# Optimization experiments

Measured on AMD Instinct MI355X. Metric: run time of the kernel, lower is better.

## Reference

```python
import jax, jax.numpy as jnp
import numpy as np

B, H, N, D = 1, 8, 2048, 64  # n >> d: fastmax's intended long-seq / small-head-dim regime


def setup_inputs() -> dict:
    key = jax.random.key(0)
    kq, kk, kv, kr = jax.random.split(key, 4)
    q = jax.random.normal(kq, (B, H, N, D), dtype=jnp.float32)
    k = jax.random.normal(kk, (B, H, N, D), dtype=jnp.float32)
    v = jax.random.normal(kv, (B, H, N, D), dtype=jnp.float32)
    rpe_matrix = jax.random.normal(kr, (2 * N - 1, D), dtype=jnp.float32)
    return {"q": q, "k": k, "v": v, "rpe_matrix": rpe_matrix, "mask": 1}


def reference(q, k, v, rpe_matrix, mask):
    # Fastmax: 2nd-order Taylor approximation of softmax attention,
    # weight(i,j) = 1 + s_ij + s_ij^2 / 2 where s_ij = q_i . (k_j) + q_i . rpe[i-j+n-1],
    # normalized by the row-sum, optionally causal (mask).
    b, h, n, d = q.shape
    # content scores: (b,h,n,n)
    s = jnp.einsum('bhid,bhjd->bhij', q, k)
    # RPE scores: project q onto every relative-position embedding, then gather
    # the (i,j) -> i-j+n-1 diagonal structure.  qr: (b,h,n,2n-1)
    qr = jnp.einsum('bhid,md->bhim', q, rpe_matrix)
    i = jnp.arange(n)[:, None]
    j = jnp.arange(n)[None, :]
    rel = i - j + (n - 1)  # (n,n) in [0, 2n-2]
    s = s + jnp.take_along_axis(qr, rel[None, None], axis=-1)
    # Taylor-2 exp approximation
    w = 1.0 + s + 0.5 * s * s
    if mask:  # causal
        w = jnp.where(j <= i, w, 0.0)
    denom = jnp.sum(w, axis=-1, keepdims=True)  # (b,h,n,1)
    out = jnp.einsum('bhij,bhjd->bhid', w, v) / denom
    return out
```

## Files before the change

### kernel.cpp

```cpp
#include <hip/hip_runtime.h>
#include <hip/hip_bf16.h>

#define HH 8
#define NN 2048
#define DD 64

typedef __attribute__((ext_vector_type(8))) short bf16x8;
typedef __attribute__((ext_vector_type(4))) float f32x4;
typedef __attribute__((ext_vector_type(8))) unsigned short u16x8;
typedef unsigned short ushort_t;

static __device__ __forceinline__ unsigned short f2bf(float x) {
    union { float f; unsigned u; } un; un.f = x;
    unsigned r = un.u + 0x7FFFu + ((un.u >> 16) & 1u);
    return (unsigned short)(r >> 16);
}
static __device__ __forceinline__ unsigned short f2bf_t(float x) {
    union { float f; unsigned u; } un; un.f = x;
    return (unsigned short)(un.u >> 16);
}
static __device__ __forceinline__ float bf2f(unsigned short u) {
    union { unsigned u; float f; } un; un.u = ((unsigned)u) << 16;
    return un.f;
}

#define OFF_Q  0u
#define OFF_K  2097152u
#define OFF_VT 4194304u
#define OFF_R  6291456u
#define OFF_P  6815744u
#define WS_NEED 11272192u

#define NQ4 262144
#define NR4 65520
#define CVT_BLOCKS 2305
__global__ void pre_kernel(const float* __restrict__ q, const float* __restrict__ k,
                           const float* __restrict__ r, const float* __restrict__ v,
                           ushort_t* __restrict__ ws) {
    __shared__ __align__(16) ushort_t T[64][72];
    if (blockIdx.x < CVT_BLOCKS) {
        int idx = blockIdx.x * 256 + threadIdx.x;
        const float* src; ushort_t* dst; int off;
        if (idx < NQ4) { src = q; dst = (ushort_t*)((char*)ws + OFF_Q); off = idx; }
        else if (idx < 2 * NQ4) { src = k; dst = (ushort_t*)((char*)ws + OFF_K); off = idx - NQ4; }
        else if (idx < 2 * NQ4 + NR4) { src = r; dst = (ushort_t*)((char*)ws + OFF_R); off = idx - 2 * NQ4; }
        else return;
        float4 f = *(const float4*)&src[4 * (size_t)off];
        ushort4 u; u.x = f2bf(f.x); u.y = f2bf(f.y); u.z = f2bf(f.z); u.w = f2bf(f.w);
        *(ushort4*)&dst[4 * (size_t)off] = u;
    } else {
        ushort_t* vt = (ushort_t*)((char*)ws + OFF_VT);
        const int bb = blockIdx.x - CVT_BLOCKS;
        const int h = bb >> 5;
        const int n0 = (bb & 31) * 64;
        const int tid = threadIdx.x;
        const float* vh = v + (size_t)h * NN * DD;
        #pragma unroll
        for (int p = 0; p < 4; ++p) {
            int c = tid + 256 * p; int rr = c >> 4, dc = (c & 15) << 2;
            float4 f = *(const float4*)&vh[(size_t)(n0 + rr) * DD + dc];
            T[dc + 0][rr] = f2bf(f.x); T[dc + 1][rr] = f2bf(f.y);
            T[dc + 2][rr] = f2bf(f.z); T[dc + 3][rr] = f2bf(f.w);
        }
        __syncthreads();
        #pragma unroll
        for (int p = 0; p < 2; ++p) {
            int c = tid + 256 * p; int d = c >> 3, nn = (c & 7) << 3;
            *(u16x8*)&vt[((size_t)h * 64 + d) * NN + n0 + nn] = *(const u16x8*)&T[d][nn];
        }
    }
}

__global__ __launch_bounds__(256, 2)
void fastmax_main(const ushort_t* __restrict__ wsb, float* __restrict__ outg,
                  float* __restrict__ wsPart)
{
    __shared__ __align__(16) ushort_t Ks[2][64][72];
    __shared__ __align__(16) ushort_t Bs[2][96][72];
    __shared__ __align__(16) ushort_t Vts[2][64][72];
    __shared__ __align__(16) unsigned char U[12800];
    float* Epi = (float*)U;

    const ushort_t* qb  = (const ushort_t*)((const char*)wsb + OFF_Q);
    const ushort_t* kb  = (const ushort_t*)((const char*)wsb + OFF_K);
    const ushort_t* vtb = (const ushort_t*)((const char*)wsb + OFF_VT);
    const ushort_t* rb_ = (const ushort_t*)((const char*)wsb + OFF_R);

    const int tid = threadIdx.x;
    const int w   = tid >> 6;
    const int l   = tid & 63;
    const int lq  = l >> 4;
    const int ln  = l & 15;
    const int rt  = w & 1;
    const int ch  = w >> 1;

    ushort_t* tsW = (ushort_t*)(U + w * 1920);
    ushort_t* wsW = (ushort_t*)(U + 7680 + w * 1280);

    const int sb     = blockIdx.x & 1;
    const int stream = blockIdx.x >> 1;
    const int head   = stream & 7;
    const int p      = stream >> 3;
    const int tileA  = 63 - p;
    const int njtA   = (tileA >> 1) + 1;
    const int tileB  = p;
    const int njtB   = (tileB >> 1) + 1;

    const ushort_t* qh  = qb  + (size_t)head * NN * DD;
    const ushort_t* kh  = kb  + (size_t)head * NN * DD;
    const ushort_t* vth = vtb + (size_t)head * DD * NN;
    float*          oh  = outg + (size_t)head * NN * DD;

    const int sw = 16 * rt - 32 * ch + 32;

    u16x8 rk0, rk1, rbA, rbB, rbC, rv0, rv1;
    const int c0r = tid >> 3,         c0d = (tid & 7) << 3;
    const int c1r = (tid + 256) >> 3, c1d = ((tid + 256) & 7) << 3;
    const int c2r = (tid + 512) >> 3, c2d = ((tid + 512) & 7) << 3;

    #pragma unroll 1
    for (int tsel = 0; tsel < 2; ++tsel) {
        if (tsel == 1 && sb == 0) break;
        const int tile = tsel ? tileB : tileA;
        const int jlo  = tsel ? 0 : (sb ? 17 : 0);
        const int jhi  = tsel ? njtB : (sb ? njtA : 17);
        const int i0   = tile * 32;

        bf16x8 qf0 = *(const bf16x8*)&qh[(size_t)(i0 + 16 * rt + ln) * DD +  0 + 8 * lq];
        bf16x8 qf1 = *(const bf16x8*)&qh[(size_t)(i0 + 16 * rt + ln) * DD + 32 + 8 * lq];

        f32x4 acc0 = {0,0,0,0}, acc1 = {0,0,0,0}, acc2 = {0,0,0,0}, acc3 = {0,0,0,0};
        float denv0 = 0.f, denv1 = 0.f, denv2 = 0.f, denv3 = 0.f;

        {
            const int j0 = jlo * 64;
            const int relbase = i0 - j0 + 1984;
            rk0 = *(const u16x8*)&kh[(size_t)(j0 + c0r) * DD + c0d];
            rk1 = *(const u16x8*)&kh[(size_t)(j0 + c1r) * DD + c1d];
            int r0 = relbase + c0r; if (r0 > 4094) r0 = 4094;
            int r1 = relbase + c1r; if (r1 > 4094) r1 = 4094;
            int r2 = relbase + c2r; if (r2 > 4094) r2 = 4094;
            rbA = *(const u16x8*)&rb_[(size_t)r0 * DD + c0d];
            rbB = *(const u16x8*)&rb_[(size_t)r1 * DD + c1d];
            rbC = *(const u16x8*)&rb_[(size_t)r2 * DD + c2d];
            rv0 = *(const u16x8*)&vth[(size_t)c0r * NN + j0 + c0d];
            rv1 = *(const u16x8*)&vth[(size_t)c1r * NN + j0 + c1d];
        }

        int buf = 0;
        for (int jt = jlo; jt < jhi; ++jt) {
            const int j0 = jt * 64;

            *(u16x8*)&Ks[buf][c0r][c0d] = rk0;
            *(u16x8*)&Ks[buf][c1r][c1d] = rk1;
            *(u16x8*)&Bs[buf][c0r][c0d] = rbA;
            *(u16x8*)&Bs[buf][c1r][c1d] = rbB;
            *(u16x8*)&Bs[buf][c2r][c2d] = rbC;
            *(u16x8*)&Vts[buf][c0r][c0d] = rv0;
            *(u16x8*)&Vts[buf][c1r][c1d] = rv1;

            if (jt + 1 < jhi) {
                const int jn = j0 + 64;
                const int relbase = i0 - jn + 1984;
                rk0 = *(const u16x8*)&kh[(size_t)(jn + c0r) * DD + c0d];
                rk1 = *(const u16x8*)&kh[(size_t)(jn + c1r) * DD + c1d];
                int r0 = relbase + c0r; if (r0 > 4094) r0 = 4094;
                int r1 = relbase + c1r; if (r1 > 4094) r1 = 4094;
                int r2 = relbase + c2r; if (r2 > 4094) r2 = 4094;
                rbA = *(const u16x8*)&rb_[(size_t)r0 * DD + c0d];
                rbB = *(const u16x8*)&rb_[(size_t)r1 * DD + c1d];
                rbC = *(const u16x8*)&rb_[(size_t)r2 * DD + c2d];
                rv0 = *(const u16x8*)&vth[(size_t)c0r * NN + jn + c0d];
                rv1 = *(const u16x8*)&vth[(size_t)c1r * NN + jn + c1d];
            }

            __syncthreads();

            f32x4 s0 = {0,0,0,0}, s1 = {0,0,0,0};
            {
                bf16x8 b00 = *(const bf16x8*)&Ks[buf][32 * ch      + ln][ 0 + 8 * lq];
                bf16x8 b01 = *(const bf16x8*)&Ks[buf][32 * ch      + ln][32 + 8 * lq];
                bf16x8 b10 = *(const bf16x8*)&Ks[buf][32 * ch + 16 + ln][ 0 + 8 * lq];
                bf16x8 b11 = *(const bf16x8*)&Ks[buf][32 * ch + 16 + ln][32 + 8 * lq];
                s0 = __builtin_amdgcn_mfma_f32_16x16x32_bf16(qf0, b00, s0, 0, 0, 0);
                s0 = __builtin_amdgcn_mfma_f32_16x16x32_bf16(qf1, b01, s0, 0, 0, 0);
                s1 = __builtin_amdgcn_mfma_f32_16x16x32_bf16(qf0, b10, s1, 0, 0, 0);
                s1 = __builtin_amdgcn_mfma_f32_16x16x32_bf16(qf1, b11, s1, 0, 0, 0);
            }

            #pragma unroll
            for (int bt = 0; bt < 3; ++bt) {
                f32x4 t = {0,0,0,0};
                bf16x8 b0 = *(const bf16x8*)&Bs[buf][sw + 16 * bt + ln][ 0 + 8 * lq];
                bf16x8 b1 = *(const bf16x8*)&Bs[buf][sw + 16 * bt + ln][32 + 8 * lq];
                t = __builtin_amdgcn_mfma_f32_16x16x32_bf16(qf0, b0, t, 0, 0, 0);
                t = __builtin_amdgcn_mfma_f32_16x16x32_bf16(qf1, b1, t, 0, 0, 0);
                ushort4 pk;
                pk.x = f2bf_t(t[0]); pk.y = f2bf_t(t[1]);
                pk.z = f2bf_t(t[2]); pk.w = f2bf_t(t[3]);
                *(ushort4*)&tsW[(16 * bt + ln) * 20 + 4 * lq] = pk;
            }

            #pragma unroll
            for (int ct = 0; ct < 2; ++ct) {
                f32x4 sv = ct ? s1 : s0;
                #pragma unroll
                for (int e = 0; e < 4; ++e) {
                    int rp = 4 * lq + e;
                    int cp = 16 * ct + ln;
                    int bw = rp - cp + 31;
                    float s = sv[e] + bf2f(tsW[bw * 20 + rp]);
                    float wv = 1.0f + s + 0.5f * s * s;
                    if (j0 + 32 * ch + cp > i0 + 16 * rt + rp) wv = 0.0f;
                    union { float f; unsigned u; } uw; uw.f = wv;
                    wsW[rp * 40 + cp] = (ushort_t)(uw.u >> 16);
                    uw.u &= 0xffff0000u;
                    if (e == 0) denv0 += uw.f; else if (e == 1) denv1 += uw.f;
                    else if (e == 2) denv2 += uw.f; else denv3 += uw.f;
                }
            }

            {
                bf16x8 af = *(const bf16x8*)&wsW[ln * 40 + 8 * lq];
                bf16x8 b;
                b = *(const bf16x8*)&Vts[buf][ 0 + ln][32 * ch + 8 * lq];
                acc0 = __builtin_amdgcn_mfma_f32_16x16x32_bf16(af, b, acc0, 0, 0, 0);
                b = *(const bf16x8*)&Vts[buf][16 + ln][32 * ch + 8 * lq];
                acc1 = __builtin_amdgcn_mfma_f32_16x16x32_bf16(af, b, acc1, 0, 0, 0);
                b = *(const bf16x8*)&Vts[buf][32 + ln][32 * ch + 8 * lq];
                acc2 = __builtin_amdgcn_mfma_f32_16x16x32_bf16(af, b, acc2, 0, 0, 0);
                b = *(const bf16x8*)&Vts[buf][48 + ln][32 * ch + 8 * lq];
                acc3 = __builtin_amdgcn_mfma_f32_16x16x32_bf16(af, b, acc3, 0, 0, 0);
            }
            buf ^= 1;
        }

        #pragma unroll
        for (int off = 1; off <= 8; off <<= 1) {
            denv0 += __shfl_xor(denv0, off);
            denv1 += __shfl_xor(denv1, off);
            denv2 += __shfl_xor(denv2, off);
            denv3 += __shfl_xor(denv3, off);
        }

        __syncthreads();
        if (ch == 0) {
            #pragma unroll
            for (int e = 0; e < 4; ++e) {
                int r = 16 * rt + 4 * lq + e;
                Epi[r * 68 +  0 + ln] = acc0[e];
                Epi[r * 68 + 16 + ln] = acc1[e];
                Epi[r * 68 + 32 + ln] = acc2[e];
                Epi[r * 68 + 48 + ln] = acc3[e];
            }
            if (ln == 0) {
                Epi[(16 * rt + 4 * lq + 0) * 68 + 64] = denv0;
                Epi[(16 * rt + 4 * lq + 1) * 68 + 64] = denv1;
                Epi[(16 * rt + 4 * lq + 2) * 68 + 64] = denv2;
                Epi[(16 * rt + 4 * lq + 3) * 68 + 64] = denv3;
            }
        }
        __syncthreads();
        if (ch == 1) {
            #pragma unroll
            for (int e = 0; e < 4; ++e) {
                int r = 16 * rt + 4 * lq + e;
                Epi[r * 68 +  0 + ln] += acc0[e];
                Epi[r * 68 + 16 + ln] += acc1[e];
                Epi[r * 68 + 32 + ln] += acc2[e];
                Epi[r * 68 + 48 + ln] += acc3[e];
            }
            if (ln == 0) {
                Epi[(16 * rt + 4 * lq + 0) * 68 + 64] += denv0;
                Epi[(16 * rt + 4 * lq + 1) * 68 + 64] += denv1;
                Epi[(16 * rt + 4 * lq + 2) * 68 + 64] += denv2;
                Epi[(16 * rt + 4 * lq + 3) * 68 + 64] += denv3;
            }
        }
        __syncthreads();
        if (tsel == 0) {
            float* dst = wsPart + ((size_t)(head * 32 + p) * 2 + sb) * (32 * 68);
            for (int idx = tid; idx < 32 * 68; idx += 256) dst[idx] = Epi[idx];
        } else {
            #pragma unroll
            for (int e2 = 0; e2 < 8; ++e2) {
                int idx = tid + 256 * e2;
                int r = idx >> 6, d = idx & 63;
                oh[(size_t)(i0 + r) * DD + d] = Epi[r * 68 + d] / Epi[r * 68 + 64];
            }
        }
    }
}

__global__ void combine_kernel(const float* __restrict__ wsPart, float* __restrict__ outg) {
    const int blk = blockIdx.x;
    const int head = blk >> 5;
    const int p = blk & 31;
    const int tileA = 63 - p;
    const float* p0 = wsPart + (size_t)blk * 2 * (32 * 68);
    const float* p1 = p0 + 32 * 68;
    float* oh = outg + (size_t)head * NN * DD;
    #pragma unroll
    for (int e2 = 0; e2 < 8; ++e2) {
        int idx = threadIdx.x + 256 * e2;
        int r = idx >> 6, d = idx & 63;
        float num = p0[r * 68 + d] + p1[r * 68 + d];
        float den = p0[r * 68 + 64] + p1[r * 68 + 64];
        oh[(size_t)(tileA * 32 + r) * DD + d] = num / den;
    }
}

__global__ __launch_bounds__(256, 2)
void fastmax_fallback(const float* __restrict__ qg0, const float* __restrict__ kg0,
                      const float* __restrict__ vg0, const float* __restrict__ rg,
                      float* __restrict__ outg)
{
    __shared__ __align__(16) ushort_t Qs[32][72];
    __shared__ __align__(16) ushort_t Ks2[64][72];
    __shared__ __align__(16) ushort_t Bs2[96][72];
    __shared__ __align__(16) ushort_t Vts2[96][72];
    __shared__ __align__(16) float    Tsf[32][97];
    __shared__ __align__(16) ushort_t Wsf[32][72];
    __shared__ float denomLds[32];

    const int tid = threadIdx.x;
    const int w = tid >> 6, l = tid & 63, lq = l >> 4, ln = l & 15;
    const int head = blockIdx.x & 7, ib = blockIdx.x >> 3;
    const int it = 63 - ib, i0 = it * 32, njt = (it >> 1) + 1;
    const float* qg = qg0 + (size_t)head * NN * DD;
    const float* kg = kg0 + (size_t)head * NN * DD;
    const float* vg = vg0 + (size_t)head * NN * DD;
    float* og = outg + (size_t)head * NN * DD;
    {
        #pragma unroll
        for (int p = 0; p < 2; ++p) {
            int c = tid + 256 * p; int r = c >> 4, dc = (c & 15) << 2;
            float4 f = *(const float4*)&qg[(size_t)(i0 + r) * DD + dc];
            ushort4 u; u.x = f2bf(f.x); u.y = f2bf(f.y); u.z = f2bf(f.z); u.w = f2bf(f.w);
            *(ushort4*)&Qs[r][dc] = u;
        }
        for (int idx = tid; idx < 32 * 72; idx += 256) {
            int rr = idx / 72, cc = idx - rr * 72;
            Vts2[64 + rr][cc] = (rr == 0) ? (ushort_t)0x3F80 : (ushort_t)0;
        }
    }
    f32x4 a0 = {0,0,0,0}, a1 = {0,0,0,0}, a2 = {0,0,0,0};
    const int pr = w & 1, rt = w & 1, cp = w >> 1;
    for (int jt = 0; jt < njt; ++jt) {
        const int j0 = jt * 64;
        __syncthreads();
        #pragma unroll
        for (int p = 0; p < 4; ++p) {
            int c = tid + 256 * p; int r = c >> 4, dc = (c & 15) << 2;
            float4 f = *(const float4*)&kg[(size_t)(j0 + r) * DD + dc];
            ushort4 u; u.x = f2bf(f.x); u.y = f2bf(f.y); u.z = f2bf(f.z); u.w = f2bf(f.w);
            *(ushort4*)&Ks2[r][dc] = u;
        }
        const int relbase = i0 - j0 + 1984;
        #pragma unroll
        for (int p = 0; p < 6; ++p) {
            int c = tid + 256 * p; int r = c >> 4, dc = (c & 15) << 2;
            int row = relbase + r; if (row > 4094) row = 4094;
            float4 f = *(const float4*)&rg[(size_t)row * DD + dc];
            ushort4 u; u.x = f2bf(f.x); u.y = f2bf(f.y); u.z = f2bf(f.z); u.w = f2bf(f.w);
            *(ushort4*)&Bs2[r][dc] = u;
        }
        #pragma unroll
        for (int p = 0; p < 4; ++p) {
            int c = tid + 256 * p; int r = c >> 4, dc = (c & 15) << 2;
            float4 f = *(const float4*)&vg[(size_t)(j0 + r) * DD + dc];
            Vts2[dc + 0][r] = f2bf(f.x); Vts2[dc + 1][r] = f2bf(f.y);
            Vts2[dc + 2][r] = f2bf(f.z); Vts2[dc + 3][r] = f2bf(f.w);
        }
        __syncthreads();
        f32x4 s0 = {0,0,0,0}, s1 = {0,0,0,0};
        #pragma unroll
        for (int ks = 0; ks < 2; ++ks) {
            bf16x8 a = *(const bf16x8*)&Qs[16 * rt + ln][32 * ks + 8 * lq];
            bf16x8 b0 = *(const bf16x8*)&Ks2[32 * cp + ln][32 * ks + 8 * lq];
            bf16x8 b1 = *(const bf16x8*)&Ks2[32 * cp + 16 + ln][32 * ks + 8 * lq];
            s0 = __builtin_amdgcn_mfma_f32_16x16x32_bf16(a, b0, s0, 0, 0, 0);
            s1 = __builtin_amdgcn_mfma_f32_16x16x32_bf16(a, b1, s1, 0, 0, 0);
        }
        #pragma unroll
        for (int kk = 0; kk < 3; ++kk) {
            int bt = (w >> 1) + 2 * kk;
            f32x4 t = {0,0,0,0};
            #pragma unroll
            for (int ks = 0; ks < 2; ++ks) {
                bf16x8 a = *(const bf16x8*)&Qs[16 * rt + ln][32 * ks + 8 * lq];
                bf16x8 b = *(const bf16x8*)&Bs2[16 * bt + ln][32 * ks + 8 * lq];
                t = __builtin_amdgcn_mfma_f32_16x16x32_bf16(a, b, t, 0, 0, 0);
            }
            #pragma unroll
            for (int e = 0; e < 4; ++e) Tsf[16 * rt + 4 * lq + e][16 * bt + ln] = t[e];
        }
        __syncthreads();
        #pragma unroll
        for (int ct2 = 0; ct2 < 2; ++ct2) {
            f32x4 sv = ct2 ? s1 : s0;
            int c_loc = 32 * cp + 16 * ct2 + ln, j = j0 + c_loc;
            #pragma unroll
            for (int e = 0; e < 4; ++e) {
                int r_loc = 16 * rt + 4 * lq + e, i = i0 + r_loc;
                float s = sv[e] + Tsf[r_loc][r_loc - c_loc + 63];
                float wv = 1.0f + s + 0.5f * s * s;
                if (j > i) wv = 0.0f;
                Wsf[r_loc][c_loc] = f2bf(wv);
            }
        }
        __syncthreads();
        {
            bf16x8 af0 = *(const bf16x8*)&Wsf[16 * pr + ln][ 0 + 8 * lq];
            bf16x8 af1 = *(const bf16x8*)&Wsf[16 * pr + ln][32 + 8 * lq];
            int pn0 = w >> 1; bf16x8 b;
            b = *(const bf16x8*)&Vts2[16 * (pn0 + 0) + ln][ 0 + 8 * lq];
            a0 = __builtin_amdgcn_mfma_f32_16x16x32_bf16(af0, b, a0, 0, 0, 0);
            b = *(const bf16x8*)&Vts2[16 * (pn0 + 0) + ln][32 + 8 * lq];
            a0 = __builtin_amdgcn_mfma_f32_16x16x32_bf16(af1, b, a0, 0, 0, 0);
            b = *(const bf16x8*)&Vts2[16 * (pn0 + 2) + ln][ 0 + 8 * lq];
            a1 = __builtin_amdgcn_mfma_f32_16x16x32_bf16(af0, b, a1, 0, 0, 0);
            b = *(const bf16x8*)&Vts2[16 * (pn0 + 2) + ln][32 + 8 * lq];
            a1 = __builtin_amdgcn_mfma_f32_16x16x32_bf16(af1, b, a1, 0, 0, 0);
            b = *(const bf16x8*)&Vts2[16 * (pn0 + 4) + ln][ 0 + 8 * lq];
            a2 = __builtin_amdgcn_mfma_f32_16x16x32_bf16(af0, b, a2, 0, 0, 0);
            b = *(const bf16x8*)&Vts2[16 * (pn0 + 4) + ln][32 + 8 * lq];
            a2 = __builtin_amdgcn_mfma_f32_16x16x32_bf16(af1, b, a2, 0, 0, 0);
        }
    }
    if (w < 2 && ln == 0) {
        #pragma unroll
        for (int e = 0; e < 4; ++e) denomLds[16 * pr + 4 * lq + e] = a2[e];
    }
    __syncthreads();
    #pragma unroll
    for (int k = 0; k < 2; ++k) {
        int pn = (w >> 1) + 2 * k;
        f32x4 acc = k ? a1 : a0;
        #pragma unroll
        for (int e = 0; e < 4; ++e) {
            int r_loc = 16 * pr + 4 * lq + e;
            og[(size_t)(i0 + r_loc) * DD + 16 * pn + ln] = acc[e] / denomLds[r_loc];
        }
    }
}

extern "C" void kernel_launch(void* const* d_in, const int* in_sizes, int n_in,
                              void* d_out, int out_size, void* d_ws, size_t ws_size,
                              hipStream_t stream) {
    const float* q   = (const float*)d_in[0];
    const float* k   = (const float*)d_in[1];
    const float* v   = (const float*)d_in[2];
    const float* rpe = (const float*)d_in[3];
    float* out = (float*)d_out;

    if (ws_size >= WS_NEED) {
        ushort_t* wsb = (ushort_t*)d_ws;
        float* wsPart = (float*)((char*)d_ws + OFF_P);
        hipLaunchKernelGGL(pre_kernel, dim3(CVT_BLOCKS + 256), dim3(256), 0, stream,
                           q, k, rpe, v, wsb);
        hipLaunchKernelGGL(fastmax_main, dim3(512), dim3(256), 0, stream,
                           wsb, out, wsPart);
        hipLaunchKernelGGL(combine_kernel, dim3(256), dim3(256), 0, stream, wsPart, out);
    } else {
        hipLaunchKernelGGL(fastmax_fallback, dim3(512), dim3(256), 0, stream,
                           q, k, v, rpe, out);
    }
}
```

Before: 103.5 us.

## Split work 4-way per stream, load K/RPE/V fragments directly from global

Removes the shared-memory staging and double-buffering of K, RPE and V tiles. MFMA B-fragments are now loaded straight from global memory, which drops the per-iteration __syncthreads and shrinks LDS use so occupancy can rise to 4 blocks per CU. Each (head, tile-pair) stream's 33 key tiles are split into 4 sub-ranges, so the grid grows to 1024 blocks. Every block writes partial numerators and denominators that an expanded combine kernel sums. The cost is redundant global/L2 traffic (no LDS reuse across waves), a larger workspace, and more partial-result writes.

```diff
diff --git a/kernel.cpp b/kernel.cpp
--- a/kernel.cpp
+++ b/kernel.cpp
@@ -29,7 +29,7 @@
 #define OFF_VT 4194304u
 #define OFF_R  6291456u
 #define OFF_P  6815744u
-#define WS_NEED 11272192u
+#define WS_NEED 24641536u
 
 #define NQ4 262144
 #define NR4 65520
@@ -71,15 +71,13 @@
     }
 }
 
-__global__ __launch_bounds__(256, 2)
+__global__ __launch_bounds__(256, 4)
 void fastmax_main(const ushort_t* __restrict__ wsb, float* __restrict__ outg,
                   float* __restrict__ wsPart)
 {
-    __shared__ __align__(16) ushort_t Ks[2][64][72];
-    __shared__ __align__(16) ushort_t Bs[2][96][72];
-    __shared__ __align__(16) ushort_t Vts[2][64][72];
     __shared__ __align__(16) unsigned char U[12800];
     float* Epi = (float*)U;
+    (void)outg;
 
     const ushort_t* qb  = (const ushort_t*)((const char*)wsb + OFF_Q);
     const ushort_t* kb  = (const ushort_t*)((const char*)wsb + OFF_K);
@@ -97,34 +95,31 @@
     ushort_t* tsW = (ushort_t*)(U + w * 1920);
     ushort_t* wsW = (ushort_t*)(U + 7680 + w * 1280);
 
-    const int sb     = blockIdx.x & 1;
-    const int stream = blockIdx.x >> 1;
-    const int head   = stream & 7;
-    const int p      = stream >> 3;
-    const int tileA  = 63 - p;
-    const int njtA   = (tileA >> 1) + 1;
-    const int tileB  = p;
-    const int njtB   = (tileB >> 1) + 1;
+    const int head = blockIdx.x & 7;
+    const int rest = blockIdx.x >> 3;
+    const int p    = rest & 31;
+    const int sub  = rest >> 5;
+    const int tileA = 63 - p;
+    const int njtA  = (tileA >> 1) + 1;
+    const int tileB = p;
+
+    const int lo = (33 * sub + 3) >> 2;
+    const int hi = (sub == 3) ? 33 : ((33 * (sub + 1) + 3) >> 2);
 
     const ushort_t* qh  = qb  + (size_t)head * NN * DD;
     const ushort_t* kh  = kb  + (size_t)head * NN * DD;
     const ushort_t* vth = vtb + (size_t)head * DD * NN;
-    float*          oh  = outg + (size_t)head * NN * DD;
 
     const int sw = 16 * rt - 32 * ch + 32;
-
-    u16x8 rk0, rk1, rbA, rbB, rbC, rv0, rv1;
-    const int c0r = tid >> 3,         c0d = (tid & 7) << 3;
-    const int c1r = (tid + 256) >> 3, c1d = ((tid + 256) & 7) << 3;
-    const int c2r = (tid + 512) >> 3, c2d = ((tid + 512) & 7) << 3;
+    const int stream = head * 32 + p;
 
     #pragma unroll 1
-    for (int tsel = 0; tsel < 2; ++tsel) {
-        if (tsel == 1 && sb == 0) break;
-        const int tile = tsel ? tileB : tileA;
-        const int jlo  = tsel ? 0 : (sb ? 17 : 0);
-        const int jhi  = tsel ? njtB : (sb ? njtA : 17);
-        const int i0   = tile * 32;
+    for (int seg = 0; seg < 2; ++seg) {
+        int tile, jlo, jhi;
+        if (seg == 0) { tile = tileA; jlo = lo; jhi = (hi < njtA) ? hi : njtA; }
+        else          { tile = tileB; jlo = (lo > njtA ? lo : njtA) - njtA; jhi = hi - njtA; }
+        if (jlo >= jhi) continue;
+        const int i0 = tile * 32;
 
         bf16x8 qf0 = *(const bf16x8*)&qh[(size_t)(i0 + 16 * rt + ln) * DD +  0 + 8 * lq];
         bf16x8 qf1 = *(const bf16x8*)&qh[(size_t)(i0 + 16 * rt + ln) * DD + 32 + 8 * lq];
@@ -132,74 +127,66 @@
         f32x4 acc0 = {0,0,0,0}, acc1 = {0,0,0,0}, acc2 = {0,0,0,0}, acc3 = {0,0,0,0};
         float denv0 = 0.f, denv1 = 0.f, denv2 = 0.f, denv3 = 0.f;
 
-        {
-            const int j0 = jlo * 64;
-            const int relbase = i0 - j0 + 1984;
-            rk0 = *(const u16x8*)&kh[(size_t)(j0 + c0r) * DD + c0d];
-            rk1 = *(const u16x8*)&kh[(size_t)(j0 + c1r) * DD + c1d];
-            int r0 = relbase + c0r; if (r0 > 4094) r0 = 4094;
-            int r1 = relbase + c1r; if (r1 > 4094) r1 = 4094;
-            int r2 = relbase + c2r; if (r2 > 4094) r2 = 4094;
-            rbA = *(const u16x8*)&rb_[(size_t)r0 * DD + c0d];
-            rbB = *(const u16x8*)&rb_[(size_t)r1 * DD + c1d];
-            rbC = *(const u16x8*)&rb_[(size_t)r2 * DD + c2d];
-            rv0 = *(const u16x8*)&vth[(size_t)c0r * NN + j0 + c0d];
-            rv1 = *(const u16x8*)&vth[(size_t)c1r * NN + j0 + c1d];
-        }
-
-        int buf = 0;
+        #pragma unroll 1
         for (int jt = jlo; jt < jhi; ++jt) {
             const int j0 = jt * 64;
-
-            *(u16x8*)&Ks[buf][c0r][c0d] = rk0;
-            *(u16x8*)&Ks[buf][c1r][c1d] = rk1;
-            *(u16x8*)&Bs[buf][c0r][c0d] = rbA;
-            *(u16x8*)&Bs[buf][c1r][c1d] = rbB;
-            *(u16x8*)&Bs[buf][c2r][c2d] = rbC;
-            *(u16x8*)&Vts[buf][c0r][c0d] = rv0;
-            *(u16x8*)&Vts[buf][c1r][c1d] = rv1;
-
-            if (jt + 1 < jhi) {
-                const int jn = j0 + 64;
-                const int relbase = i0 - jn + 1984;
-                rk0 = *(const u16x8*)&kh[(size_t)(jn + c0r) * DD + c0d];
-                rk1 = *(const u16x8*)&kh[(size_t)(jn + c1r) * DD + c1d];
-                int r0 = relbase + c0r; if (r0 > 4094) r0 = 4094;
-                int r1 = relbase + c1r; if (r1 > 4094) r1 = 4094;
-                int r2 = relbase + c2r; if (r2 > 4094) r2 = 4094;
-                rbA = *(const u16x8*)&rb_[(size_t)r0 * DD + c0d];
-                rbB = *(const u16x8*)&rb_[(size_t)r1 * DD + c1d];
-                rbC = *(const u16x8*)&rb_[(size_t)r2 * DD + c2d];
-                rv0 = *(const u16x8*)&vth[(size_t)c0r * NN + jn + c0d];
-                rv1 = *(const u16x8*)&vth[(size_t)c1r * NN + jn + c1d];
-            }
-
-            __syncthreads();
+            const int relbase = i0 - j0 + 1984;
+
+            const ushort_t* kp = kh + (size_t)(j0 + 32 * ch + ln) * DD + 8 * lq;
+            bf16x8 b00 = *(const bf16x8*)(kp);
+            bf16x8 b01 = *(const bf16x8*)(kp + 32);
+            bf16x8 b10 = *(const bf16x8*)(kp + 16 * DD);
+            bf16x8 b11 = *(const bf16x8*)(kp + 16 * DD + 32);
+
+            int br0 = relbase + sw      + ln; if (br0 > 4094) br0 = 4094;
+            int br1 = relbase + sw + 16 + ln; if (br1 > 4094) br1 = 4094;
+            int br2 = relbase + sw + 32 + ln; if (br2 > 4094) br2 = 4094;
+            const ushort_t* bp0 = rb_ + (size_t)br0 * DD + 8 * lq;
+            const ushort_t* bp1 = rb_ + (size_t)br1 * DD + 8 * lq;
+            const ushort_t* bp2 = rb_ + (size_t)br2 * DD + 8 * lq;
+            bf16x8 e0a = *(const bf16x8*)(bp0);
+            bf16x8 e0b = *(const bf16x8*)(bp0 + 32);
+            bf16x8 e1a = *(const bf16x8*)(bp1);
+            bf16x8 e1b = *(const bf16x8*)(bp1 + 32);
+            bf16x8 e2a = *(const bf16x8*)(bp2);
+            bf16x8 e2b = *(const bf16x8*)(bp2 + 32);
 
             f32x4 s0 = {0,0,0,0}, s1 = {0,0,0,0};
+            s0 = __builtin_amdgcn_mfma_f32_16x16x32_bf16(qf0, b00, s0, 0, 0, 0);
+            s0 = __builtin_amdgcn_mfma_f32_16x16x32_bf16(qf1, b01, s0, 0, 0, 0);
+            s1 = __builtin_amdgcn_mfma_f32_16x16x32_bf16(qf0, b10, s1, 0, 0, 0);
+            s1 = __builtin_amdgcn_mfma_f32_16x16x32_bf16(qf1, b11, s1, 0, 0, 0);
+
             {
-                bf16x8 b00 = *(const bf16x8*)&Ks[buf][32 * ch      + ln][ 0 + 8 * lq];
-                bf16x8 b01 = *(const bf16x8*)&Ks[buf][32 * ch      + ln][32 + 8 * lq];
-                bf16x8 b10 = *(const bf16x8*)&Ks[buf][32 * ch + 16 + ln][ 0 + 8 * lq];
-                bf16x8 b11 = *(const bf16x8*)&Ks[buf][32 * ch + 16 + ln][32 + 8 * lq];
-                s0 = __builtin_amdgcn_mfma_f32_16x16x32_bf16(qf0, b00, s0, 0, 0, 0);
-                s0 = __builtin_amdgcn_mfma_f32_16x16x32_bf16(qf1, b01, s0, 0, 0, 0);
-                s1 = __builtin_amdgcn_mfma_f32_16x16x32_bf16(qf0, b10, s1, 0, 0, 0);
-                s1 = __builtin_amdgcn_mfma_f32_16x16x32_bf16(qf1, b11, s1, 0, 0, 0);
-            }
-
-            #pragma unroll
-            for (int bt = 0; bt < 3; ++bt) {
                 f32x4 t = {0,0,0,0};
-                bf16x8 b0 = *(const bf16x8*)&Bs[buf][sw + 16 * bt + ln][ 0 + 8 * lq];
-                bf16x8 b1 = *(const bf16x8*)&Bs[buf][sw + 16 * bt + ln][32 + 8 * lq];
-                t = __builtin_amdgcn_mfma_f32_16x16x32_bf16(qf0, b0, t, 0, 0, 0);
-                t = __builtin_amdgcn_mfma_f32_16x16x32_bf16(qf1, b1, t, 0, 0, 0);
+                t = __builtin_amdgcn_mfma_f32_16x16x32_bf16(qf0, e0a, t, 0, 0, 0);
+                t = __builtin_amdgcn_mfma_f32_16x16x32_bf16(qf1, e0b, t, 0, 0, 0);
                 ushort4 pk;
-                pk.x = f2bf_t(t[0]); pk.y = f2bf_t(t[1]);
-                pk.z = f2bf_t(t[2]); pk.w = f2bf_t(t[3]);
-                *(ushort4*)&tsW[(16 * bt + ln) * 20 + 4 * lq] = pk;
-            }
+                pk.x = f2bf_t(t[0]); pk.y = f2bf_t(t[1]); pk.z = f2bf_t(t[2]); pk.w = f2bf_t(t[3]);
+                *(ushort4*)&tsW[(ln) * 20 + 4 * lq] = pk;
+            }
+            {
+                f32x4 t = {0,0,0,0};
+                t = __builtin_amdgcn_mfma_f32_16x16x32_bf16(qf0, e1a, t, 0, 0, 0);
+                t = __builtin_amdgcn_mfma_f32_16x16x32_bf16(qf1, e1b, t, 0, 0, 0);
+                ushort4 pk;
+                pk.x = f2bf_t(t[0]); pk.y = f2bf_t(t[1]); pk.z = f2bf_t(t[2]); pk.w = f2bf_t(t[3]);
+                *(ushort4*)&tsW[(16 + ln) * 20 + 4 * lq] = pk;
+            }
+            {
+                f32x4 t = {0,0,0,0};
+                t = __builtin_amdgcn_mfma_f32_16x16x32_bf16(qf0, e2a, t, 0, 0, 0);
+                t = __builtin_amdgcn_mfma_f32_16x16x32_bf16(qf1, e2b, t, 0, 0, 0);
+                ushort4 pk;
+                pk.x = f2bf_t(t[0]); pk.y = f2bf_t(t[1]); pk.z = f2bf_t(t[2]); pk.w = f2bf_t(t[3]);
+                *(ushort4*)&tsW[(32 + ln) * 20 + 4 * lq] = pk;
+            }
+
+            const ushort_t* vp = vth + (size_t)ln * NN + j0 + 32 * ch + 8 * lq;
+            bf16x8 v0 = *(const bf16x8*)(vp);
+            bf16x8 v1 = *(const bf16x8*)(vp + (size_t)16 * NN);
+            bf16x8 v2 = *(const bf16x8*)(vp + (size_t)32 * NN);
+            bf16x8 v3 = *(const bf16x8*)(vp + (size_t)48 * NN);
 
             #pragma unroll
             for (int ct = 0; ct < 2; ++ct) {
@@ -222,17 +209,11 @@
 
             {
                 bf16x8 af = *(const bf16x8*)&wsW[ln * 40 + 8 * lq];
-                bf16x8 b;
-                b = *(const bf16x8*)&Vts[buf][ 0 + ln][32 * ch + 8 * lq];
-                acc0 = __builtin_amdgcn_mfma_f32_16x16x32_bf16(af, b, acc0, 0, 0, 0);
-                b = *(const bf16x8*)&Vts[buf][16 + ln][32 * ch + 8 * lq];
-                acc1 = __builtin_amdgcn_mfma_f32_16x16x32_bf16(af, b, acc1, 0, 0, 0);
-                b = *(const bf16x8*)&Vts[buf][32 + ln][32 * ch + 8 * lq];
-                acc2 = __builtin_amdgcn_mfma_f32_16x16x32_bf16(af, b, acc2, 0, 0, 0);
-                b = *(const bf16x8*)&Vts[buf][48 + ln][32 * ch + 8 * lq];
-                acc3 = __builtin_amdgcn_mfma_f32_16x16x32_bf16(af, b, acc3, 0, 0, 0);
-            }
-            buf ^= 1;
+                acc0 = __builtin_amdgcn_mfma_f32_16x16x32_bf16(af, v0, acc0, 0, 0, 0);
+                acc1 = __builtin_amdgcn_mfma_f32_16x16x32_bf16(af, v1, acc1, 0, 0, 0);
+                acc2 = __builtin_amdgcn_mfma_f32_16x16x32_bf16(af, v2, acc2, 0, 0, 0);
+                acc3 = __builtin_amdgcn_mfma_f32_16x16x32_bf16(af, v3, acc3, 0, 0, 0);
+            }
         }
 
         #pragma unroll
@@ -278,17 +259,11 @@
             }
         }
         __syncthreads();
-        if (tsel == 0) {
-            float* dst = wsPart + ((size_t)(head * 32 + p) * 2 + sb) * (32 * 68);
+        {
+            float* dst = wsPart + ((size_t)((stream * 2 + seg) * 4 + sub)) * (32 * 68);
             for (int idx = tid; idx < 32 * 68; idx += 256) dst[idx] = Epi[idx];
-        } else {
-            #pragma unroll
-            for (int e2 = 0; e2 < 8; ++e2) {
-                int idx = tid + 256 * e2;
-                int r = idx >> 6, d = idx & 63;
-                oh[(size_t)(i0 + r) * DD + d] = Epi[r * 68 + d] / Epi[r * 68 + 64];
-            }
-        }
+        }
+        __syncthreads();
     }
 }
 
@@ -296,17 +271,34 @@
     const int blk = blockIdx.x;
     const int head = blk >> 5;
     const int p = blk & 31;
-    const int tileA = 63 - p;
-    const float* p0 = wsPart + (size_t)blk * 2 * (32 * 68);
-    const float* p1 = p0 + 32 * 68;
+    const int njtA = ((63 - p) >> 1) + 1;
     float* oh = outg + (size_t)head * NN * DD;
-    #pragma unroll
-    for (int e2 = 0; e2 < 8; ++e2) {
-        int idx = threadIdx.x + 256 * e2;
-        int r = idx >> 6, d = idx & 63;
-        float num = p0[r * 68 + d] + p1[r * 68 + d];
-        float den = p0[r * 68 + 64] + p1[r * 68 + 64];
-        oh[(size_t)(tileA * 32 + r) * DD + d] = num / den;
+    #pragma unroll 1
+    for (int tsel = 0; tsel < 2; ++tsel) {
+        const int tile = tsel ? p : (63 - p);
+        const float* base = wsPart + ((size_t)(blk * 2 + tsel)) * 4 * (32 * 68);
+        int vmask = 0;
+        #pragma unroll
+        for (int s = 0; s < 4; ++s) {
+            int lo_s = (33 * s + 3) >> 2;
+            int hi_s = (s == 3) ? 33 : ((33 * (s + 1) + 3) >> 2);
+            bool valid = tsel ? (hi_s > njtA) : (lo_s < njtA);
+            if (valid) vmask |= 1 << s;
+        }
+        #pragma unroll
+        for (int e2 = 0; e2 < 8; ++e2) {
+            int idx = threadIdx.x + 256 * e2;
+            int r = idx >> 6, d = idx & 63;
+            float num = 0.f, den = 0.f;
+            #pragma unroll
+            for (int s = 0; s < 4; ++s) {
+                if (vmask & (1 << s)) {
+                    num += base[s * 2176 + r * 68 + d];
+                    den += base[s * 2176 + r * 68 + 64];
+                }
+            }
+            oh[(size_t)(tile * 32 + r) * DD + d] = num / den;
+        }
     }
 }
 
@@ -459,7 +451,7 @@
         float* wsPart = (float*)((char*)d_ws + OFF_P);
         hipLaunchKernelGGL(pre_kernel, dim3(CVT_BLOCKS + 256), dim3(256), 0, stream,
                            q, k, rpe, v, wsb);
-        hipLaunchKernelGGL(fastmax_main, dim3(512), dim3(256), 0, stream,
+        hipLaunchKernelGGL(fastmax_main, dim3(1024), dim3(256), 0, stream,
                            wsb, out, wsPart);
         hipLaunchKernelGGL(combine_kernel, dim3(256), dim3(256), 0, stream, wsPart, out);
     } else {
```

Measured after the change: 143.4 us. +38.5%, slower.
